# Optimization experiments

Measured on AMD Instinct MI355X. Metric: run time of the kernel, lower is better.

The kernel has to match this reference:

```python
import jax, jax.numpy as jnp
import numpy as np

B, S, E, H, VP, L, T = 256, 256, 1024, 1024, 8, 64, 16


def setup_inputs() -> dict:
    key = jax.random.key(0)
    ks = jax.random.split(key, 10)
    image = jax.random.normal(ks[0], (B, S, E), jnp.float32)
    view_position = jax.random.uniform(ks[1], (B, VP), jnp.float32)
    label = (jax.random.uniform(ks[2], (B, T + 1, L)) > 0.5).astype(jnp.float32)
    # lengths sorted descending (length_sorted_rnn decorator), max forced to T+1
    length = jnp.sort(jax.random.randint(ks[3], (B,), 2, T + 2))[::-1]
    length = length.at[0].set(T + 1)
    def lin(k, out_d, in_d):
        return jax.random.normal(k, (out_d, in_d), jnp.float32) * (1.0 / np.sqrt(in_d)).astype(np.float32)
    IN = E + VP + 1 + L  # 1097: lstm_sizes = [embedding, view_position, 1, label]
    FC_OUT = L + H + 1 + 1  # 1090: fc_sizes = [label, hidden, 1, 1]
    return {
        'image': image, 'view_position': view_position, 'label': label, 'length': length,
        'W_h': lin(ks[4], H, E), 'b_h': jnp.zeros((H,), jnp.float32),
        'W_m': lin(ks[5], H, E), 'b_m': jnp.zeros((H,), jnp.float32),
        'W_ih': lin(ks[6], 4 * H, IN), 'W_hh': lin(ks[7], 4 * H, H),
        'b_ih': jnp.zeros((4 * H,), jnp.float32), 'b_hh': jnp.zeros((4 * H,), jnp.float32),
        'W_fc': lin(ks[8], FC_OUT, H), 'b_fc': jnp.zeros((FC_OUT,), jnp.float32),
    }


def reference(image, view_position, label, length, W_h, b_h, W_m, b_m,
              W_ih, W_hh, b_ih, b_hh, W_fc, b_fc):
    # Dropout is identity (inference). image: (B,S,E)
    image_mean = image.mean(axis=1)                      # (B,E)
    h0 = jnp.tanh(image_mean @ W_h.T + b_h)              # (B,H)
    m0 = jnp.tanh(image_mean @ W_m.T + b_m)              # (B,H)
    n_steps = label.shape[1] - 1
    bsz = image_mean.shape[0]

    def step(carry, inp):
        h, m = carry
        lab_t, t = inp
        begin = jnp.where(t == 0, 1.0, 0.0) * jnp.ones((bsz, 1), image_mean.dtype)
        x = jnp.concatenate([image_mean, view_position, begin, lab_t], axis=1)  # (B, 1097)
        gates = x @ W_ih.T + b_ih + h @ W_hh.T + b_hh    # (B, 4H)
        i, f, g, o = jnp.split(gates, 4, axis=1)
        m2 = jax.nn.sigmoid(f) * m + jax.nn.sigmoid(i) * jnp.tanh(g)
        h2 = jax.nn.sigmoid(o) * jnp.tanh(m2)
        out = h2 @ W_fc.T + b_fc                         # (B, L+H+2)
        topic = jax.nn.relu(out[:, L:L + H])
        stop = jax.nn.sigmoid(out[:, L + H:L + H + 1])
        temp = jnp.exp(out[:, L + H + 1:])
        return (h2, m2), jnp.concatenate([topic, stop, temp], axis=1)

    labels_tm = jnp.swapaxes(label[:, :n_steps], 0, 1)   # (T,B,L) time-major
    _, outs = jax.lax.scan(step, (h0, m0), (labels_tm, jnp.arange(n_steps)))
    # pad_sequence semantics: entries with t >= length-1 are zero padding
    mask = (jnp.arange(n_steps)[:, None] < (length - 1)[None, :]).astype(outs.dtype)
    return outs * mask[:, :, None]                       # (T, B, H+2) = [topic|stop|temp]
```

## Files before the change

### kernel.cpp

```cpp
#include <hip/hip_runtime.h>
#include <stdint.h>

typedef unsigned short u16;
typedef __attribute__((ext_vector_type(8))) short v8s;
typedef __attribute__((ext_vector_type(4))) float v4f;

__device__ __forceinline__ u16 f2bf(float f) {
  uint32_t x = __float_as_uint(f);
  return (u16)((x + 0x7fffu + ((x >> 16) & 1u)) >> 16);
}
__device__ __forceinline__ float bf2f(u16 u) {
  return __uint_as_float(((uint32_t)u) << 16);
}
__device__ __forceinline__ float sigf(float x) { return 1.f / (1.f + __expf(-x)); }
__device__ __forceinline__ float tanhf_fast(float x) {
  float e = __expf(-2.f * fabsf(x));
  float r = (1.f - e) / (1.f + e);
  return copysignf(r, x);
}

__device__ __forceinline__ v4f mfma16(v8s a, v8s b, v4f c) {
  return __builtin_amdgcn_mfma_f32_16x16x32_bf16(a, b, c, 0, 0, 0);
}

__device__ __forceinline__ void gll16(const u16* src, u16* ldsdst) {
  __builtin_amdgcn_global_load_lds(
      reinterpret_cast<__attribute__((address_space(1))) uint32_t*>(
          reinterpret_cast<uintptr_t>(src)),
      reinterpret_cast<__attribute__((address_space(3))) uint32_t*>(
          reinterpret_cast<uintptr_t>(ldsdst)),
      16, 0, 0);
}

__device__ __forceinline__ size_t fpoff(int row, int k, int KT) {
  return ((size_t)(((row >> 4) * KT + (k >> 6)) * 2 + ((k >> 5) & 1)) * 64 +
          ((k >> 3) & 3) * 16 + (row & 15)) * 8 + (k & 7);
}

__device__ __forceinline__ void load8(const float* p, float* f) {
  float4 a = *(const float4*)p;
  float4 b = *(const float4*)(p + 4);
  f[0]=a.x; f[1]=a.y; f[2]=a.z; f[3]=a.w; f[4]=b.x; f[5]=b.y; f[6]=b.z; f[7]=b.w;
}
__device__ __forceinline__ void store8bf(u16* dst, const float* f) {
  u16 t[8];
#pragma unroll
  for (int i = 0; i < 8; ++i) t[i] = f2bf(f[i]);
  *(v8s*)dst = *(const v8s*)t;
}

__global__ __launch_bounds__(256) void k_convert_mean(
    const float* __restrict__ Wh, const float* __restrict__ Wm,
    const float* __restrict__ Wih, const float* __restrict__ Whh,
    const float* __restrict__ Wfc, const float* __restrict__ label,
    const float* __restrict__ image,
    u16* __restrict__ wcomb, u16* __restrict__ whhb, u16* __restrict__ wfcb,
    u16* __restrict__ wlabb, u16* __restrict__ labb,
    float4* __restrict__ pacc, unsigned* __restrict__ ctr) {
  const int bid = blockIdx.x, tid = threadIdx.x;
  if (bid >= 8000) {
    ctr[(bid - 8000) * 256 + tid] = 0u;
    return;
  }
  if (bid >= 5952) {
    int bi = bid - 5952;
    int b = bi >> 3, oct = bi & 7;
    const float4* src =
        (const float4*)image + (size_t)b * 65536 + (size_t)oct * 32 * 256 + tid;
    float4 s = make_float4(0.f, 0.f, 0.f, 0.f);
#pragma unroll 8
    for (int ss = 0; ss < 32; ++ss) {
      float4 v = src[(size_t)ss * 256];
      s.x += v.x; s.y += v.y; s.z += v.z; s.w += v.w;
    }
    pacc[(size_t)bi * 256 + tid] = s;
    return;
  }
  int64_t u = (int64_t)bid * 256 + tid;
  float f[8];
  if (u < 786432) {
    int lu = (int)u;
    int r15 = lu & 15, q = (lu >> 4) & 3, s = (lu >> 6) & 1, tile = lu >> 7;
    int tk = tile & 15, tr = tile >> 4;
    int row = tr * 16 + r15, k = tk * 64 + s * 32 + q * 8;
    if (row < 1024) load8(Wh + (size_t)row * 1024 + k, f);
    else if (row < 2048) load8(Wm + (size_t)(row - 1024) * 1024 + k, f);
    else {
      const float* p = Wih + (size_t)(row - 2048) * 1097 + k;
#pragma unroll
      for (int i = 0; i < 8; ++i) f[i] = p[i];
    }
    store8bf(wcomb + (size_t)lu * 8, f);
  } else if (u < 1310720) {
    int lu = (int)(u - 786432);
    int r15 = lu & 15, q = (lu >> 4) & 3, s = (lu >> 6) & 1, tile = lu >> 7;
    int tk = tile & 15, tr = tile >> 4;
    int row = tr * 16 + r15, k = tk * 64 + s * 32 + q * 8;
    load8(Whh + (size_t)row * 1024 + k, f);
    store8bf(whhb + (size_t)lu * 8, f);
  } else if (u < 1458176) {
    int lu = (int)(u - 1310720);
    int r15 = lu & 15, q = (lu >> 4) & 3, s = (lu >> 6) & 1, tile = lu >> 7;
    int tk = tile & 15, tr = tile >> 4;
    int row = tr * 16 + r15, k = tk * 64 + s * 32 + q * 8;
    if (row < 1090) load8(Wfc + (size_t)row * 1024 + k, f);
    else {
#pragma unroll
      for (int i = 0; i < 8; ++i) f[i] = 0.f;
    }
    store8bf(wfcb + (size_t)lu * 8, f);
  } else if (u < 1490944) {
    int lu = (int)(u - 1458176);
    int r15 = lu & 15, q = (lu >> 4) & 3, s = (lu >> 6) & 1, tile = lu >> 7;
    int row = tile * 16 + r15, k = s * 32 + q * 8;
    const float* p = Wih + (size_t)row * 1097 + 1033 + k;
#pragma unroll
    for (int i = 0; i < 8; ++i) f[i] = p[i];
    store8bf(wlabb + (size_t)lu * 8, f);
  } else {
    int lu = (int)(u - 1490944);
    int r15 = lu & 15, q = (lu >> 4) & 3, s = (lu >> 6) & 1, tile = lu >> 7;
    int row = tile * 16 + r15, k = s * 32 + q * 8;
    int t = row >> 8, b = row & 255;
    load8(label + ((size_t)b * 17 + t) * 64 + k, f);
    store8bf(labb + (size_t)lu * 8, f);
  }
}

__global__ __launch_bounds__(256) void k_mean2(const float4* __restrict__ pacc,
                                               u16* __restrict__ meanbf) {
  int b = blockIdx.x, tid = threadIdx.x;
  float4 s = make_float4(0.f, 0.f, 0.f, 0.f);
#pragma unroll
  for (int q = 0; q < 8; ++q) {
    float4 v = pacc[((size_t)b * 8 + q) * 256 + tid];
    s.x += v.x; s.y += v.y; s.z += v.z; s.w += v.w;
  }
  const float inv = 1.f / 256.f;
  int k = tid * 4;
  ushort4 o;
  o.x = f2bf(s.x * inv); o.y = f2bf(s.y * inv);
  o.z = f2bf(s.z * inv); o.w = f2bf(s.w * inv);
  *(ushort4*)&meanbf[fpoff(b, k, 16)] = o;
}

__global__ __launch_bounds__(256) void k_gemm_init(
    const u16* __restrict__ meanbf, const u16* __restrict__ wcomb,
    const float* __restrict__ bh, const float* __restrict__ bm,
    const float* __restrict__ bih, const float* __restrict__ bhh,
    const float* __restrict__ vp, const float* __restrict__ Wih,
    u16* __restrict__ hbuf, float* __restrict__ mbuf, float* __restrict__ basebuf) {
  __shared__ alignas(16) u16 lA[4 * 1024];
  __shared__ alignas(16) u16 lB[4 * 1024];
  const int tid = threadIdx.x, lane = tid & 63, wid = tid >> 6;
  const int bm0 = (blockIdx.x & 3) * 64;
  const int bn0 = (blockIdx.x >> 2) * 64;
  const int wr = wid >> 1, wc = wid & 1;
  v4f acc[2][2];
#pragma unroll
  for (int i = 0; i < 2; ++i)
#pragma unroll
    for (int j = 0; j < 2; ++j) acc[i][j] = (v4f){0.f, 0.f, 0.f, 0.f};

  for (int kt = 0; kt < 16; ++kt) {
    const u16* asrc = meanbf + ((size_t)((bm0 >> 4) + wid) * 16 + kt) * 1024 + lane * 8;
    gll16(asrc, lA + wid * 1024);
    gll16(asrc + 512, lA + wid * 1024 + 512);
    const u16* bsrc = wcomb + ((size_t)((bn0 >> 4) + wid) * 16 + kt) * 1024 + lane * 8;
    gll16(bsrc, lB + wid * 1024);
    gll16(bsrc + 512, lB + wid * 1024 + 512);
    __syncthreads();
#pragma unroll
    for (int s = 0; s < 2; ++s) {
      v8s a0 = *(const v8s*)&lA[(size_t)(wr * 2) * 1024 + s * 512 + lane * 8];
      v8s a1 = *(const v8s*)&lA[(size_t)(wr * 2 + 1) * 1024 + s * 512 + lane * 8];
      v8s b0 = *(const v8s*)&lB[(size_t)(wc * 2) * 1024 + s * 512 + lane * 8];
      v8s b1 = *(const v8s*)&lB[(size_t)(wc * 2 + 1) * 1024 + s * 512 + lane * 8];
      acc[0][0] = mfma16(a0, b0, acc[0][0]);
      acc[0][1] = mfma16(a0, b1, acc[0][1]);
      acc[1][0] = mfma16(a1, b0, acc[1][0]);
      acc[1][1] = mfma16(a1, b1, acc[1][1]);
    }
    __syncthreads();
  }
#pragma unroll
  for (int fm = 0; fm < 2; ++fm)
#pragma unroll
    for (int fn = 0; fn < 2; ++fn)
#pragma unroll
      for (int rg = 0; rg < 4; ++rg) {
        int row = bm0 + wr * 32 + fm * 16 + ((lane >> 4) << 2) + rg;
        int col = bn0 + wc * 32 + fn * 16 + (lane & 15);
        float v = acc[fm][fn][rg];
        if (col < 1024) {
          hbuf[fpoff(row, col, 16)] = f2bf(tanhf_fast(v + bh[col]));
        } else if (col < 2048) {
          int nn = col - 1024;
          mbuf[(size_t)row * 1024 + nn] = tanhf_fast(v + bm[nn]);
        } else {
          int j = col - 2048;
          float sv = v + bih[j] + bhh[j];
#pragma unroll
          for (int q = 0; q < 8; ++q)
            sv += vp[row * 8 + q] * Wih[(size_t)j * 1097 + 1024 + q];
          basebuf[(size_t)row * 4096 + j] = sv;
        }
      }
}

__global__ __launch_bounds__(256, 1) void k_steps(
    const u16* __restrict__ whhb, const u16* __restrict__ wlabb,
    const u16* __restrict__ labb, const float* __restrict__ basebuf,
    const float* __restrict__ Wih, const float* __restrict__ mbuf,
    u16* __restrict__ hbuf, unsigned* __restrict__ ctr) {
  __shared__ alignas(16) u16 lA[64 * 512];
  __shared__ alignas(16) u16 lLab[64 * 512];
  __shared__ alignas(16) float lact[4][32 * 33];
  const int tid = threadIdx.x, lane = tid & 63, wid = tid >> 6;
  const int blk = blockIdx.x;
  const int grp = blk & 7;
  const int n0idx = blk >> 3;
  const int n0 = n0idx * 32;
  const int b0 = grp * 32;
  const int atr = b0 >> 4;

#pragma unroll
  for (int j = 0; j < 16; ++j) {
    const int c = wid * 16 + j;
    const int t = c >> 2, i = (c >> 1) & 1, s = c & 1;
    gll16(labb + (size_t)(t * 16 + atr + i) * 1024 + s * 512 + lane * 8,
          lLab + c * 512);
  }

  const int tr0 = wid * 64 + (n0 >> 4);
  v8s breg[16][2][2];
#pragma unroll
  for (int kt = 0; kt < 16; ++kt)
#pragma unroll
    for (int s = 0; s < 2; ++s)
#pragma unroll
      for (int j = 0; j < 2; ++j)
        breg[kt][s][j] =
            *(const v8s*)&whhb[((size_t)(tr0 + j) * 16 + kt) * 1024 + s * 512 + lane * 8];
  v8s wlreg[2][2];
#pragma unroll
  for (int s = 0; s < 2; ++s)
#pragma unroll
    for (int j = 0; j < 2; ++j)
      wlreg[s][j] = *(const v8s*)&wlabb[(size_t)(tr0 + j) * 1024 + s * 512 + lane * 8];

  const int rowm = tid >> 3;
  const int nql = (tid & 7) * 4;
  const int b = b0 + rowm;
  const int n = n0 + nql;
  float4 mreg = *(const float4*)&mbuf[(size_t)b * 1024 + n];
  float4 bse[4], wbv[4];
#pragma unroll
  for (int g = 0; g < 4; ++g) {
    bse[g] = *(const float4*)&basebuf[(size_t)b * 4096 + g * 1024 + n];
#pragma unroll
    for (int q = 0; q < 4; ++q)
      ((float*)&wbv[g])[q] = Wih[(size_t)(g * 1024 + n + q) * 1097 + 1032];
  }
  __syncthreads();

  for (int t = 0; t < 16; ++t) {
    if (t > 0) {
      if (wid == 0) {
        const unsigned* f = &ctr[((t - 1) * 8 + grp) * 32];
        for (int it = 0; it < (1 << 18); ++it) {
          unsigned v = __hip_atomic_load(&f[lane & 31], __ATOMIC_RELAXED,
                                         __HIP_MEMORY_SCOPE_AGENT);
          if (__ballot(v == 0u) == 0ull) break;
          __builtin_amdgcn_s_sleep(2);
        }
      }
      __syncthreads();
    }
    const u16* hsrc = hbuf + (size_t)t * 262144;
    __builtin_amdgcn_sched_barrier(0);
#pragma unroll
    for (int j = 0; j < 8; ++j) {
      const int hc = wid * 8 + j;
      const int i = hc >> 4, kt = (hc >> 1) & 7, s = hc & 1;
      gll16(hsrc + ((size_t)(atr + i) * 16 + kt) * 1024 + s * 512 + lane * 8,
            lA + (i * 32 + kt * 2 + s) * 512);
    }
    __builtin_amdgcn_sched_barrier(0);
#pragma unroll
    for (int j = 0; j < 8; ++j) {
      const int hc = wid * 8 + j;
      const int i = hc >> 4, kt = ((hc >> 1) & 7) + 8, s = hc & 1;
      gll16(hsrc + ((size_t)(atr + i) * 16 + kt) * 1024 + s * 512 + lane * 8,
            lA + (i * 32 + kt * 2 + s) * 512);
    }
    __builtin_amdgcn_sched_barrier(0);

    v4f acc[2][2];
#pragma unroll
    for (int i = 0; i < 2; ++i)
#pragma unroll
      for (int j = 0; j < 2; ++j) acc[i][j] = (v4f){0.f, 0.f, 0.f, 0.f};
#pragma unroll
    for (int s = 0; s < 2; ++s) {
      v8s aL0 = *(const v8s*)&lLab[(size_t)(t * 4 + 0 * 2 + s) * 512 + lane * 8];
      v8s aL1 = *(const v8s*)&lLab[(size_t)(t * 4 + 1 * 2 + s) * 512 + lane * 8];
      acc[0][0] = mfma16(aL0, wlreg[s][0], acc[0][0]);
      acc[0][1] = mfma16(aL0, wlreg[s][1], acc[0][1]);
      acc[1][0] = mfma16(aL1, wlreg[s][0], acc[1][0]);
      acc[1][1] = mfma16(aL1, wlreg[s][1], acc[1][1]);
    }

    __builtin_amdgcn_sched_barrier(0);
    asm volatile("s_waitcnt vmcnt(8)" ::: "memory");
    __builtin_amdgcn_sched_barrier(0);
    __builtin_amdgcn_s_barrier();
    __builtin_amdgcn_sched_barrier(0);
#pragma unroll
    for (int kt = 0; kt < 8; ++kt)
#pragma unroll
      for (int s = 0; s < 2; ++s) {
        v8s a0 = *(const v8s*)&lA[(size_t)((0 * 16 + kt) * 2 + s) * 512 + lane * 8];
        v8s a1 = *(const v8s*)&lA[(size_t)((1 * 16 + kt) * 2 + s) * 512 + lane * 8];
        acc[0][0] = mfma16(a0, breg[kt][s][0], acc[0][0]);
        acc[0][1] = mfma16(a0, breg[kt][s][1], acc[0][1]);
        acc[1][0] = mfma16(a1, breg[kt][s][0], acc[1][0]);
        acc[1][1] = mfma16(a1, breg[kt][s][1], acc[1][1]);
      }

    __builtin_amdgcn_sched_barrier(0);
    asm volatile("s_waitcnt vmcnt(0)" ::: "memory");
    __builtin_amdgcn_sched_barrier(0);
    __builtin_amdgcn_s_barrier();
    __builtin_amdgcn_sched_barrier(0);
#pragma unroll
    for (int kt = 8; kt < 16; ++kt)
#pragma unroll
      for (int s = 0; s < 2; ++s) {
        v8s a0 = *(const v8s*)&lA[(size_t)((0 * 16 + kt) * 2 + s) * 512 + lane * 8];
        v8s a1 = *(const v8s*)&lA[(size_t)((1 * 16 + kt) * 2 + s) * 512 + lane * 8];
        acc[0][0] = mfma16(a0, breg[kt][s][0], acc[0][0]);
        acc[0][1] = mfma16(a0, breg[kt][s][1], acc[0][1]);
        acc[1][0] = mfma16(a1, breg[kt][s][0], acc[1][0]);
        acc[1][1] = mfma16(a1, breg[kt][s][1], acc[1][1]);
      }

#pragma unroll
    for (int fm = 0; fm < 2; ++fm)
#pragma unroll
      for (int fn = 0; fn < 2; ++fn)
#pragma unroll
        for (int rg = 0; rg < 4; ++rg) {
          int rr = fm * 16 + ((lane >> 4) << 2) + rg;
          int cc = fn * 16 + (lane & 15);
          lact[wid][rr * 33 + cc] = acc[fm][fn][rg];
        }
    __syncthreads();

    const float w0 = (t == 0) ? 1.f : 0.f;
    float m2a[4];
    u16 h2a[4];
#pragma unroll
    for (int q = 0; q < 4; ++q) {
      float gi = lact[0][rowm * 33 + nql + q] + ((const float*)&bse[0])[q] + w0 * ((const float*)&wbv[0])[q];
      float gf = lact[1][rowm * 33 + nql + q] + ((const float*)&bse[1])[q] + w0 * ((const float*)&wbv[1])[q];
      float gg = lact[2][rowm * 33 + nql + q] + ((const float*)&bse[2])[q] + w0 * ((const float*)&wbv[2])[q];
      float go = lact[3][rowm * 33 + nql + q] + ((const float*)&bse[3])[q] + w0 * ((const float*)&wbv[3])[q];
      float mov = ((const float*)&mreg)[q];
      float m2 = sigf(gf) * mov + sigf(gi) * tanhf_fast(gg);
      float h2 = sigf(go) * tanhf_fast(m2);
      m2a[q] = m2;
      h2a[q] = f2bf(h2);
    }
    mreg = make_float4(m2a[0], m2a[1], m2a[2], m2a[3]);
    ushort4 ho;
    ho.x = h2a[0]; ho.y = h2a[1]; ho.z = h2a[2]; ho.w = h2a[3];
    unsigned long long hv;
    __builtin_memcpy(&hv, &ho, 8);
    __hip_atomic_store(
        reinterpret_cast<unsigned long long*>(
            &hbuf[(size_t)(t + 1) * 262144 + fpoff(b, n, 16)]),
        hv, __ATOMIC_RELAXED, __HIP_MEMORY_SCOPE_AGENT);

    if (t < 15) {
      __syncthreads();
      if (tid == 0)
        __hip_atomic_store(&ctr[(t * 8 + grp) * 32 + n0idx], 1u,
                           __ATOMIC_RELAXED, __HIP_MEMORY_SCOPE_AGENT);
    }
  }
}

__global__ __launch_bounds__(256) void k_fc(
    const u16* __restrict__ hall, const u16* __restrict__ wfcb,
    const float* __restrict__ bfc, const int* __restrict__ length,
    float* __restrict__ out) {
  __shared__ alignas(16) u16 lA[4 * 1024];
  __shared__ alignas(16) u16 lB[4 * 1024];
  const int tid = threadIdx.x, lane = tid & 63, wid = tid >> 6;
  const int bm0 = (int)(blockIdx.x % 64) * 64;
  const int bn0 = (int)(blockIdx.x / 64) * 64;
  const int wr = wid >> 1, wc = wid & 1;
  v4f acc[2][2];
#pragma unroll
  for (int i = 0; i < 2; ++i)
#pragma unroll
    for (int j = 0; j < 2; ++j) acc[i][j] = (v4f){0.f, 0.f, 0.f, 0.f};

  for (int kt = 0; kt < 16; ++kt) {
    const u16* asrc = hall + ((size_t)((bm0 >> 4) + wid) * 16 + kt) * 1024 + lane * 8;
    gll16(asrc, lA + wid * 1024);
    gll16(asrc + 512, lA + wid * 1024 + 512);
    const u16* bsrc = wfcb + ((size_t)((bn0 >> 4) + wid) * 16 + kt) * 1024 + lane * 8;
    gll16(bsrc, lB + wid * 1024);
    gll16(bsrc + 512, lB + wid * 1024 + 512);
    __syncthreads();
#pragma unroll
    for (int s = 0; s < 2; ++s) {
      v8s a0 = *(const v8s*)&lA[(size_t)(wr * 2) * 1024 + s * 512 + lane * 8];
      v8s a1 = *(const v8s*)&lA[(size_t)(wr * 2 + 1) * 1024 + s * 512 + lane * 8];
      v8s b0 = *(const v8s*)&lB[(size_t)(wc * 2) * 1024 + s * 512 + lane * 8];
      v8s b1 = *(const v8s*)&lB[(size_t)(wc * 2 + 1) * 1024 + s * 512 + lane * 8];
      acc[0][0] = mfma16(a0, b0, acc[0][0]);
      acc[0][1] = mfma16(a0, b1, acc[0][1]);
      acc[1][0] = mfma16(a1, b0, acc[1][0]);
      acc[1][1] = mfma16(a1, b1, acc[1][1]);
    }
    __syncthreads();
  }
#pragma unroll
  for (int fm = 0; fm < 2; ++fm)
#pragma unroll
    for (int fn = 0; fn < 2; ++fn)
#pragma unroll
      for (int rg = 0; rg < 4; ++rg) {
        int r = bm0 + wr * 32 + fm * 16 + ((lane >> 4) << 2) + rg;
        int j = bn0 + wc * 32 + fn * 16 + (lane & 15);
        if (j < 64 || j >= 1090) continue;
        int t = r >> 8, b = r & 255;
        float v = acc[fm][fn][rg] + bfc[j];
        int c;
        if (j < 1088) { c = j - 64; v = fmaxf(v, 0.f); }
        else if (j == 1088) { c = 1024; v = 1.f / (1.f + expf(-v)); }
        else { c = 1025; v = expf(v); }
        if (t >= length[b] - 1) v = 0.f;
        out[((size_t)t * 256 + b) * 1026 + c] = v;
      }
}

extern "C" void kernel_launch(void* const* d_in, const int* in_sizes, int n_in,
                              void* d_out, int out_size, void* d_ws, size_t ws_size,
                              hipStream_t stream) {
  (void)in_sizes; (void)n_in; (void)out_size; (void)ws_size;
  const float* image  = (const float*)d_in[0];
  const float* vp     = (const float*)d_in[1];
  const float* label  = (const float*)d_in[2];
  const int*   length = (const int*)d_in[3];
  const float* Wh  = (const float*)d_in[4];
  const float* bh  = (const float*)d_in[5];
  const float* Wm  = (const float*)d_in[6];
  const float* bm  = (const float*)d_in[7];
  const float* Wih = (const float*)d_in[8];
  const float* Whh = (const float*)d_in[9];
  const float* bih = (const float*)d_in[10];
  const float* bhh = (const float*)d_in[11];
  const float* Wfc = (const float*)d_in[12];
  const float* bfc = (const float*)d_in[13];
  float* out = (float*)d_out;
  char* ws = (char*)d_ws;

  size_t off = 0;
  u16* wcomb  = (u16*)(ws + off); off += (size_t)6144 * 1024 * 2;
  u16* whhb   = (u16*)(ws + off); off += (size_t)4096 * 1024 * 2;
  u16* wfcb   = (u16*)(ws + off); off += (size_t)1152 * 1024 * 2;
  u16* wlabb  = (u16*)(ws + off); off += (size_t)4096 * 64 * 2;
  u16* labb   = (u16*)(ws + off); off += (size_t)4096 * 64 * 2;
  u16* meanbf = (u16*)(ws + off); off += (size_t)256 * 1024 * 2;
  u16* hbuf   = (u16*)(ws + off); off += (size_t)17 * 256 * 1024 * 2;
  float* mbuf    = (float*)(ws + off); off += (size_t)256 * 1024 * 4;
  float* basebuf = (float*)(ws + off); off += (size_t)256 * 4096 * 4;
  unsigned* ctr = (unsigned*)(ws + off); off += 4096 * 4;
  float4* pacc = (float4*)(ws + off); off += (size_t)2048 * 256 * 16;

  k_convert_mean<<<8016, 256, 0, stream>>>(Wh, Wm, Wih, Whh, Wfc, label, image,
                                           wcomb, whhb, wfcb, wlabb, labb, pacc, ctr);
  k_mean2<<<256, 256, 0, stream>>>(pacc, meanbf);
  k_gemm_init<<<384, 256, 0, stream>>>(meanbf, wcomb, bh, bm, bih, bhh, vp, Wih,
                                       hbuf, mbuf, basebuf);
  k_steps<<<256, 256, 0, stream>>>(whhb, wlabb, labb, basebuf, Wih, mbuf, hbuf, ctr);
  k_fc<<<1152, 256, 0, stream>>>(hbuf + (size_t)256 * 1024, wfcb, bfc, length, out);
}
```

Measured before the change: 195.6 us.

## Map batch groups to XCDs dynamically and relax step-barrier atomics

Each block reads its hardware XCC id and takes a slot from a per-XCC atomic counter, so every batch group of 32 blocks that exchanges h state is placed on one XCD and shares its L2. The spin-wait and flag/h stores switch from agent-scope atomics to volatile plain accesses, and the sleep interval is shortened. This aims to cut cross-XCD coherence latency in the per-step barrier. The scheme assumes exactly 32 blocks land on each XCD and that the counter region is zeroed. Without release/acquire ordering, the plain stores could also become visible out of order.

```diff
diff --git a/kernel.cpp b/kernel.cpp
--- a/kernel.cpp
+++ b/kernel.cpp
@@ -216,10 +216,22 @@
   __shared__ alignas(16) u16 lA[64 * 512];
   __shared__ alignas(16) u16 lLab[64 * 512];
   __shared__ alignas(16) float lact[4][32 * 33];
+  __shared__ int sGrp, sSlot;
   const int tid = threadIdx.x, lane = tid & 63, wid = tid >> 6;
-  const int blk = blockIdx.x;
-  const int grp = blk & 7;
-  const int n0idx = blk >> 3;
+
+  if (tid == 0) {
+    unsigned xcc;
+    asm volatile("s_getreg_b32 %0, hwreg(20, 0, 32)" : "=s"(xcc));
+    xcc &= 7u;
+    unsigned slot = __hip_atomic_fetch_add(&ctr[3840 + xcc], 1u,
+                                           __ATOMIC_RELAXED,
+                                           __HIP_MEMORY_SCOPE_AGENT);
+    sGrp = (int)xcc;
+    sSlot = (int)(slot & 31u);
+  }
+  __syncthreads();
+  const int grp = sGrp;
+  const int n0idx = sSlot;
   const int n0 = n0idx * 32;
   const int b0 = grp * 32;
   const int atr = b0 >> 4;
@@ -267,12 +279,11 @@
   for (int t = 0; t < 16; ++t) {
     if (t > 0) {
       if (wid == 0) {
-        const unsigned* f = &ctr[((t - 1) * 8 + grp) * 32];
+        const volatile unsigned* f = &ctr[((t - 1) * 8 + grp) * 32];
         for (int it = 0; it < (1 << 18); ++it) {
-          unsigned v = __hip_atomic_load(&f[lane & 31], __ATOMIC_RELAXED,
-                                         __HIP_MEMORY_SCOPE_AGENT);
+          unsigned v = f[lane & 31];
           if (__ballot(v == 0u) == 0ull) break;
-          __builtin_amdgcn_s_sleep(2);
+          __builtin_amdgcn_s_sleep(1);
         }
       }
       __syncthreads();
@@ -377,16 +388,15 @@
     ho.x = h2a[0]; ho.y = h2a[1]; ho.z = h2a[2]; ho.w = h2a[3];
     unsigned long long hv;
     __builtin_memcpy(&hv, &ho, 8);
-    __hip_atomic_store(
-        reinterpret_cast<unsigned long long*>(
-            &hbuf[(size_t)(t + 1) * 262144 + fpoff(b, n, 16)]),
-        hv, __ATOMIC_RELAXED, __HIP_MEMORY_SCOPE_AGENT);
+    *reinterpret_cast<unsigned long long*>(
+        &hbuf[(size_t)(t + 1) * 262144 + fpoff(b, n, 16)]) = hv;
 
     if (t < 15) {
       __syncthreads();
-      if (tid == 0)
-        __hip_atomic_store(&ctr[(t * 8 + grp) * 32 + n0idx], 1u,
-                           __ATOMIC_RELAXED, __HIP_MEMORY_SCOPE_AGENT);
+      if (tid == 0) {
+        volatile unsigned* fw = &ctr[(t * 8 + grp) * 32 + n0idx];
+        *fw = 1u;
+      }
     }
   }
 }
```

Measured after the change: 202.7 us. 3.6% more time.
